# Performance work log

Hardware: AMD Instinct MI355X
Metric: run time of the kernel (lower is better)

Reference implementation:

```python
import jax, jax.numpy as jnp
import numpy as np

N_NODES = 10000
N_EDGES = 50000
DIM = 32
NHEAD = 4
HEAD_DIM = DIM // NHEAD
LN_EPS = 1e-5


def setup_inputs() -> dict:
    key = jax.random.key(0)
    ks = jax.random.split(key, 16)
    E, N, H, HD, D = N_EDGES, N_NODES, NHEAD, HEAD_DIM, DIM
    s = 1.0 / np.sqrt(D)
    return {
        "in_feat": jax.random.normal(ks[0], (N, D), jnp.float32),
        "src": jax.random.randint(ks[1], (E,), 0, N, jnp.int32),
        "dst": jax.random.randint(ks[2], (E,), 0, N, jnp.int32),
        "src_key_w": jax.random.normal(ks[3], (E, H, HD, D), jnp.float32) * s,
        "dst_key_w": jax.random.normal(ks[4], (E, H, HD, D), jnp.float32) * s,
        "src_key_b": jax.random.normal(ks[5], (E, H, HD), jnp.float32) * 0.02,
        "dst_key_b": jax.random.normal(ks[6], (E, H, HD), jnp.float32) * 0.02,
        "src_value_w": jax.random.normal(ks[7], (E, H, HD, D), jnp.float32) * s,
        "dst_value_w": jax.random.normal(ks[8], (E, H, HD, D), jnp.float32) * s,
        "src_value_b": jax.random.normal(ks[9], (E, H, HD), jnp.float32) * 0.02,
        "dst_value_b": jax.random.normal(ks[10], (E, H, HD), jnp.float32) * 0.02,
        "query": jax.random.normal(ks[11], (N, H, HD), jnp.float32) * s,
        "node_w": jax.random.normal(ks[12], (N, D, D), jnp.float32) * s,
        "node_b": jax.random.normal(ks[13], (N, D), jnp.float32) * 0.02,
        "ln_w": jnp.ones((D,), jnp.float32),
        "ln_b": jnp.zeros((D,), jnp.float32),
    }


def _layernorm(x, w, b):
    mu = jnp.mean(x, axis=-1, keepdims=True)
    var = jnp.mean(jnp.square(x - mu), axis=-1, keepdims=True)
    return (x - mu) * jax.lax.rsqrt(var + LN_EPS) * w + b


def reference(in_feat, src, dst, src_key_w, dst_key_w, src_key_b, dst_key_b,
              src_value_w, dst_value_w, src_value_b, dst_value_b,
              query, node_w, node_b, ln_w, ln_b):
    N = in_feat.shape[0]
    E = src.shape[0]
    u = in_feat[src]          # (E, D) source node feature per edge
    v = in_feat[dst]          # (E, D) destination node feature per edge

    # edgewise dynamic-weight linear: per-edge hypernetwork matmuls
    K = (jnp.einsum('ehdi,ei->ehd', src_key_w, u) + src_key_b
         + jnp.einsum('ehdi,ei->ehd', dst_key_w, v) + dst_key_b)   # (E, H, HD)
    V = (jnp.einsum('ehdi,ei->ehd', src_value_w, u) + src_value_b
         + jnp.einsum('ehdi,ei->ehd', dst_value_w, v) + dst_value_b)  # (E, H, HD)

    # e_dot_v(KEY, QUERY): per-edge per-head dot with dst-node query
    logits = jnp.einsum('ehd,ehd->eh', K, query[dst])  # (E, H)

    # edge_softmax over incoming edges of each dst node, per head
    m = jax.ops.segment_max(logits, dst, num_segments=N)   # (N, H)
    ex = jnp.exp(logits - m[dst])
    denom = jax.ops.segment_sum(ex, dst, num_segments=N)   # (N, H)
    attn = ex / denom[dst]                                  # (E, H)

    # weighted scatter-sum aggregation into dst nodes
    agg = jax.ops.segment_sum(V * attn[..., None], dst, num_segments=N)  # (N, H, HD)
    agg = agg.reshape(N, -1)  # (N, D)

    # nodewise dynamic linear + relu
    out = jnp.einsum('noi,ni->no', node_w, agg) + node_b
    out = jax.nn.relu(out)

    # residual + layernorm
    out = _layernorm(in_feat + out, ln_w, ln_b)

    key_feat = K.reshape(E, -1)
    value_feat = V.reshape(E, -1)
    return out, key_feat, value_feat, attn
```

## Files before the change

### kernel.cpp

```cpp
#include <hip/hip_runtime.h>
#include <math.h>

constexpr int N = 10000;
constexpr int E = 50000;
constexpr int D = 32;
constexpr int H = 4;

typedef float v4f __attribute__((ext_vector_type(4)));

__global__ __launch_bounds__(256) void hist_kernel(const int* __restrict__ dst,
                                                   int* __restrict__ counts)
{
    const int e = blockIdx.x * 256 + threadIdx.x;
    if (e < E) atomicAdd(counts + dst[e], 1);
}

__global__ __launch_bounds__(1024) void scan_kernel(const int* __restrict__ counts,
                                                    int* __restrict__ offsets,
                                                    int* __restrict__ cursor)
{
    __shared__ int part[1024];
    const int t = threadIdx.x;
    constexpr int PER = (N + 1023) / 1024;
    const int base = t * PER;
    int loc[PER];
    int s = 0;
    #pragma unroll
    for (int i = 0; i < PER; ++i) {
        const int c = (base + i < N) ? counts[base + i] : 0;
        loc[i] = s;
        s += c;
    }
    part[t] = s;
    __syncthreads();
    for (int off = 1; off < 1024; off <<= 1) {
        const int v = (t >= off) ? part[t - off] : 0;
        __syncthreads();
        part[t] += v;
        __syncthreads();
    }
    const int pre = (t == 0) ? 0 : part[t - 1];
    #pragma unroll
    for (int i = 0; i < PER; ++i) {
        if (base + i < N) {
            const int o = pre + loc[i];
            offsets[base + i] = o;
            cursor[base + i]  = o;
        }
    }
    if (t == 0) offsets[N] = E;
}

__global__ __launch_bounds__(256) void scatter_kernel(const int* __restrict__ dst,
                                                      int* __restrict__ cursor,
                                                      int* __restrict__ edge_list)
{
    const int e = blockIdx.x * 256 + threadIdx.x;
    if (e < E) {
        const int p = atomicAdd(cursor + dst[e], 1);
        edge_list[p] = e;
    }
}

__global__ __launch_bounds__(256) void edge_kernel(
    const float* __restrict__ in_feat,
    const int*   __restrict__ src, const int* __restrict__ dst,
    const float* __restrict__ skw, const float* __restrict__ dkw,
    const float* __restrict__ skb, const float* __restrict__ dkb,
    const float* __restrict__ svw, const float* __restrict__ dvw,
    const float* __restrict__ svb, const float* __restrict__ dvb,
    const float* __restrict__ query,
    float* __restrict__ key_feat, float* __restrict__ value_feat,
    float* __restrict__ ex_out)
{
    const int e   = blockIdx.x;
    const int tid = threadIdx.x;
    const int hd  = tid >> 3;
    const int seg = tid & 7;
    const int s = src[e];
    const int d = dst[e];

    const float4 u4 = *reinterpret_cast<const float4*>(in_feat + s * D + seg * 4);
    const float4 v4 = *reinterpret_cast<const float4*>(in_feat + d * D + seg * 4);

    const size_t woff = (size_t)e * 1024 + (size_t)tid * 4;
    const v4f wa = __builtin_nontemporal_load(reinterpret_cast<const v4f*>(skw + woff));
    const v4f wb = __builtin_nontemporal_load(reinterpret_cast<const v4f*>(dkw + woff));
    const v4f wc = __builtin_nontemporal_load(reinterpret_cast<const v4f*>(svw + woff));
    const v4f wd = __builtin_nontemporal_load(reinterpret_cast<const v4f*>(dvw + woff));

    float pk = wa.x * u4.x + wa.y * u4.y + wa.z * u4.z + wa.w * u4.w
             + wb.x * v4.x + wb.y * v4.y + wb.z * v4.z + wb.w * v4.w;
    float pv = wc.x * u4.x + wc.y * u4.y + wc.z * u4.z + wc.w * u4.w
             + wd.x * v4.x + wd.y * v4.y + wd.z * v4.z + wd.w * v4.w;

    #pragma unroll
    for (int off = 1; off < 8; off <<= 1) {
        pk += __shfl_xor(pk, off);
        pv += __shfl_xor(pv, off);
    }

    const int bi = e * D + hd;
    float c = 0.0f;
    if (seg == 0) {
        const float Kv = pk + skb[bi] + dkb[bi];
        const float Vv = pv + svb[bi] + dvb[bi];
        key_feat[bi]   = Kv;
        value_feat[bi] = Vv;
        c = Kv * query[d * D + hd];
    }
    #pragma unroll
    for (int off = 8; off < 64; off <<= 1) c += __shfl_xor(c, off);

    if ((tid & 63) == 0) {
        const int h = tid >> 6;
        ex_out[e * H + h] = expf(c);
    }
}

__global__ __launch_bounds__(256) void node_kernel(
    const int*   __restrict__ offsets, const int* __restrict__ edge_list,
    const float* __restrict__ in_feat, const float* __restrict__ value_feat,
    const float* __restrict__ node_w,  const float* __restrict__ node_b,
    const float* __restrict__ ln_w,    const float* __restrict__ ln_b,
    float* __restrict__ attn,
    float* __restrict__ out)
{
    __shared__ float agg_sh[4][33];
    const int wave = threadIdx.x >> 6;
    const int lane = threadIdx.x & 63;
    const int n = blockIdx.x * 4 + wave;

    const int beg = offsets[n];
    const int deg = offsets[n + 1] - beg;

    const int slot = lane >> 2;
    const int hh   = lane & 3;
    const int hd   = lane & 31;
    const int h    = hd >> 3;

    float ds = 0.0f;
    for (int k = slot; k < deg; k += 16)
        ds += attn[edge_list[beg + k] * H + hh];
    #pragma unroll
    for (int off = 4; off < 64; off <<= 1) ds += __shfl_xor(ds, off);
    const float rden = (ds != 0.0f) ? 1.0f / ds : 0.0f;

    float aggv = 0.0f;
    for (int c = 0; c < deg; c += 16) {
        const int rem = (deg - c < 16) ? (deg - c) : 16;
        int   ee = 0;
        float a  = 0.0f;
        if (slot < rem) {
            ee = edge_list[beg + c + slot];
            const int idx = ee * H + hh;
            a = attn[idx] * rden;
            attn[idx] = a;
        }
        for (int kk = 0; kk < rem; ++kk) {
            const float ak = __shfl(a, kk * 4 + h);
            const int  ek = __shfl(ee, kk * 4);
            aggv += value_feat[ek * D + hd] * ak;
        }
    }
    agg_sh[wave][hd] = aggv;
    __syncthreads();

    const int o = lane >> 1, half = lane & 1;
    const float* w = node_w + (size_t)n * 1024 + o * 32 + half * 16;
    const float* g = &agg_sh[wave][half * 16];
    float p = 0.0f;
    #pragma unroll
    for (int j = 0; j < 16; j += 4) {
        const float4 wv = *reinterpret_cast<const float4*>(w + j);
        p += wv.x * g[j] + wv.y * g[j + 1] + wv.z * g[j + 2] + wv.w * g[j + 3];
    }
    p += __shfl_xor(p, 1);

    const float r = in_feat[n * D + o] + fmaxf(p + node_b[n * D + o], 0.0f);

    float sum = r, sq = r * r;
    #pragma unroll
    for (int off = 2; off < 64; off <<= 1) {
        sum += __shfl_xor(sum, off);
        sq  += __shfl_xor(sq, off);
    }
    const float mean = sum * (1.0f / 32.0f);
    const float var  = sq * (1.0f / 32.0f) - mean * mean;
    const float y = (r - mean) * rsqrtf(var + 1e-5f) * ln_w[o] + ln_b[o];
    if (half == 0) out[n * D + o] = y;
}

extern "C" void kernel_launch(void* const* d_in, const int* in_sizes, int n_in,
                              void* d_out, int out_size, void* d_ws, size_t ws_size,
                              hipStream_t stream)
{
    const float* in_feat = (const float*)d_in[0];
    const int*   src     = (const int*)d_in[1];
    const int*   dst     = (const int*)d_in[2];
    const float* skw     = (const float*)d_in[3];
    const float* dkw     = (const float*)d_in[4];
    const float* skb     = (const float*)d_in[5];
    const float* dkb     = (const float*)d_in[6];
    const float* svw     = (const float*)d_in[7];
    const float* dvw     = (const float*)d_in[8];
    const float* svb     = (const float*)d_in[9];
    const float* dvb     = (const float*)d_in[10];
    const float* query   = (const float*)d_in[11];
    const float* node_w  = (const float*)d_in[12];
    const float* node_b  = (const float*)d_in[13];
    const float* ln_w    = (const float*)d_in[14];
    const float* ln_b    = (const float*)d_in[15];

    float* out        = (float*)d_out;
    float* key_feat   = out + (size_t)N * D;
    float* value_feat = key_feat + (size_t)E * D;
    float* attn       = value_feat + (size_t)E * D;

    int* counts    = (int*)d_ws;
    int* offsets   = counts + N;
    int* cursor    = offsets + (N + 1);
    int* edge_list = cursor + N;

    hipMemsetAsync(counts, 0, (size_t)N * sizeof(int), stream);
    hist_kernel<<<(E + 255) / 256, 256, 0, stream>>>(dst, counts);
    scan_kernel<<<1, 1024, 0, stream>>>(counts, offsets, cursor);
    scatter_kernel<<<(E + 255) / 256, 256, 0, stream>>>(dst, cursor, edge_list);

    edge_kernel<<<E, 256, 0, stream>>>(in_feat, src, dst,
                                       skw, dkw, skb, dkb,
                                       svw, dvw, svb, dvb,
                                       query, key_feat, value_feat, attn);

    node_kernel<<<N / 4, 256, 0, stream>>>(offsets, edge_list,
                                           in_feat, value_feat,
                                           node_w, node_b, ln_w, ln_b,
                                           attn, out);
}
```

Measured before the change: 705.3 us.

## Replace CSR build and gather with atomic scatter aggregation in edge kernel

The edge kernel now atomically accumulates exp(logit)*V into a per-node aggregation buffer (aliased onto the output region) and accumulates the softmax denominators per node and head. This removes the histogram, scan and scatter kernels and the per-node gather loop over incoming edges. Normalisation moves into the node kernel (dividing the aggregate by the denominator) and into a new small elementwise kernel that divides the stored attention weights. The trade-off is many float atomics to scattered destination nodes, plus summation order that is no longer deterministic.

```diff
diff --git a/kernel.cpp b/kernel.cpp
--- a/kernel.cpp
+++ b/kernel.cpp
@@ -8,60 +8,6 @@
 
 typedef float v4f __attribute__((ext_vector_type(4)));
 
-__global__ __launch_bounds__(256) void hist_kernel(const int* __restrict__ dst,
-                                                   int* __restrict__ counts)
-{
-    const int e = blockIdx.x * 256 + threadIdx.x;
-    if (e < E) atomicAdd(counts + dst[e], 1);
-}
-
-__global__ __launch_bounds__(1024) void scan_kernel(const int* __restrict__ counts,
-                                                    int* __restrict__ offsets,
-                                                    int* __restrict__ cursor)
-{
-    __shared__ int part[1024];
-    const int t = threadIdx.x;
-    constexpr int PER = (N + 1023) / 1024;
-    const int base = t * PER;
-    int loc[PER];
-    int s = 0;
-    #pragma unroll
-    for (int i = 0; i < PER; ++i) {
-        const int c = (base + i < N) ? counts[base + i] : 0;
-        loc[i] = s;
-        s += c;
-    }
-    part[t] = s;
-    __syncthreads();
-    for (int off = 1; off < 1024; off <<= 1) {
-        const int v = (t >= off) ? part[t - off] : 0;
-        __syncthreads();
-        part[t] += v;
-        __syncthreads();
-    }
-    const int pre = (t == 0) ? 0 : part[t - 1];
-    #pragma unroll
-    for (int i = 0; i < PER; ++i) {
-        if (base + i < N) {
-            const int o = pre + loc[i];
-            offsets[base + i] = o;
-            cursor[base + i]  = o;
-        }
-    }
-    if (t == 0) offsets[N] = E;
-}
-
-__global__ __launch_bounds__(256) void scatter_kernel(const int* __restrict__ dst,
-                                                      int* __restrict__ cursor,
-                                                      int* __restrict__ edge_list)
-{
-    const int e = blockIdx.x * 256 + threadIdx.x;
-    if (e < E) {
-        const int p = atomicAdd(cursor + dst[e], 1);
-        edge_list[p] = e;
-    }
-}
-
 __global__ __launch_bounds__(256) void edge_kernel(
     const float* __restrict__ in_feat,
     const int*   __restrict__ src, const int* __restrict__ dst,
@@ -71,7 +17,9 @@
     const float* __restrict__ svb, const float* __restrict__ dvb,
     const float* __restrict__ query,
     float* __restrict__ key_feat, float* __restrict__ value_feat,
-    float* __restrict__ ex_out)
+    float* __restrict__ ex_out,
+    float* __restrict__ aggU,
+    float* __restrict__ denom)
 {
     const int e   = blockIdx.x;
     const int tid = threadIdx.x;
@@ -101,10 +49,11 @@
     }
 
     const int bi = e * D + hd;
-    float c = 0.0f;
+    float c  = 0.0f;
+    float Vv = 0.0f;
     if (seg == 0) {
         const float Kv = pk + skb[bi] + dkb[bi];
-        const float Vv = pv + svb[bi] + dvb[bi];
+        Vv = pv + svb[bi] + dvb[bi];
         key_feat[bi]   = Kv;
         value_feat[bi] = Vv;
         c = Kv * query[d * D + hd];
@@ -112,18 +61,21 @@
     #pragma unroll
     for (int off = 8; off < 64; off <<= 1) c += __shfl_xor(c, off);
 
-    if ((tid & 63) == 0) {
-        const int h = tid >> 6;
-        ex_out[e * H + h] = expf(c);
+    if (seg == 0) {
+        const float ex = expf(c);
+        atomicAdd(aggU + d * D + hd, ex * Vv);
+        if ((tid & 63) == 0) {
+            const int h = tid >> 6;
+            ex_out[e * H + h] = ex;
+            atomicAdd(denom + d * H + h, ex);
+        }
     }
 }
 
 __global__ __launch_bounds__(256) void node_kernel(
-    const int*   __restrict__ offsets, const int* __restrict__ edge_list,
-    const float* __restrict__ in_feat, const float* __restrict__ value_feat,
+    const float* __restrict__ in_feat, const float* __restrict__ denom,
     const float* __restrict__ node_w,  const float* __restrict__ node_b,
     const float* __restrict__ ln_w,    const float* __restrict__ ln_b,
-    float* __restrict__ attn,
     float* __restrict__ out)
 {
     __shared__ float agg_sh[4][33];
@@ -131,39 +83,12 @@
     const int lane = threadIdx.x & 63;
     const int n = blockIdx.x * 4 + wave;
 
-    const int beg = offsets[n];
-    const int deg = offsets[n + 1] - beg;
+    const int hd = lane & 31;
+    const int h  = hd >> 3;
 
-    const int slot = lane >> 2;
-    const int hh   = lane & 3;
-    const int hd   = lane & 31;
-    const int h    = hd >> 3;
-
-    float ds = 0.0f;
-    for (int k = slot; k < deg; k += 16)
-        ds += attn[edge_list[beg + k] * H + hh];
-    #pragma unroll
-    for (int off = 4; off < 64; off <<= 1) ds += __shfl_xor(ds, off);
+    const float ds   = denom[n * H + h];
     const float rden = (ds != 0.0f) ? 1.0f / ds : 0.0f;
-
-    float aggv = 0.0f;
-    for (int c = 0; c < deg; c += 16) {
-        const int rem = (deg - c < 16) ? (deg - c) : 16;
-        int   ee = 0;
-        float a  = 0.0f;
-        if (slot < rem) {
-            ee = edge_list[beg + c + slot];
-            const int idx = ee * H + hh;
-            a = attn[idx] * rden;
-            attn[idx] = a;
-        }
-        for (int kk = 0; kk < rem; ++kk) {
-            const float ak = __shfl(a, kk * 4 + h);
-            const int  ek = __shfl(ee, kk * 4);
-            aggv += value_feat[ek * D + hd] * ak;
-        }
-    }
-    agg_sh[wave][hd] = aggv;
+    agg_sh[wave][hd] = out[n * D + hd] * rden;
     __syncthreads();
 
     const int o = lane >> 1, half = lane & 1;
@@ -189,6 +114,24 @@
     const float var  = sq * (1.0f / 32.0f) - mean * mean;
     const float y = (r - mean) * rsqrtf(var + 1e-5f) * ln_w[o] + ln_b[o];
     if (half == 0) out[n * D + o] = y;
+}
+
+__global__ __launch_bounds__(256) void attn_kernel(
+    const int* __restrict__ dst, const float* __restrict__ denom,
+    float* __restrict__ attn)
+{
+    const int e = blockIdx.x * 256 + threadIdx.x;
+    if (e < E) {
+        const int d = dst[e];
+        const float4 ex = *reinterpret_cast<const float4*>(attn + (size_t)e * H);
+        const float4 dn = *reinterpret_cast<const float4*>(denom + (size_t)d * H);
+        float4 r;
+        r.x = ex.x / dn.x;
+        r.y = ex.y / dn.y;
+        r.z = ex.z / dn.z;
+        r.w = ex.w / dn.w;
+        *reinterpret_cast<float4*>(attn + (size_t)e * H) = r;
+    }
 }
 
 extern "C" void kernel_launch(void* const* d_in, const int* in_sizes, int n_in,
@@ -217,23 +160,19 @@
     float* value_feat = key_feat + (size_t)E * D;
     float* attn       = value_feat + (size_t)E * D;
 
-    int* counts    = (int*)d_ws;
-    int* offsets   = counts + N;
-    int* cursor    = offsets + (N + 1);
-    int* edge_list = cursor + N;
+    float* denom = (float*)d_ws;
 
-    hipMemsetAsync(counts, 0, (size_t)N * sizeof(int), stream);
-    hist_kernel<<<(E + 255) / 256, 256, 0, stream>>>(dst, counts);
-    scan_kernel<<<1, 1024, 0, stream>>>(counts, offsets, cursor);
-    scatter_kernel<<<(E + 255) / 256, 256, 0, stream>>>(dst, cursor, edge_list);
+    hipMemsetAsync(out,   0, (size_t)N * D * sizeof(float), stream);
+    hipMemsetAsync(denom, 0, (size_t)N * H * sizeof(float), stream);
 
     edge_kernel<<<E, 256, 0, stream>>>(in_feat, src, dst,
                                        skw, dkw, skb, dkb,
                                        svw, dvw, svb, dvb,
-                                       query, key_feat, value_feat, attn);
+                                       query, key_feat, value_feat, attn,
+                                       out, denom);
 
-    node_kernel<<<N / 4, 256, 0, stream>>>(offsets, edge_list,
-                                           in_feat, value_feat,
-                                           node_w, node_b, ln_w, ln_b,
-                                           attn, out);
+    node_kernel<<<N / 4, 256, 0, stream>>>(in_feat, denom,
+                                           node_w, node_b, ln_w, ln_b, out);
+
+    attn_kernel<<<(E + 255) / 256, 256, 0, stream>>>(dst, denom, attn);
 }
```

Result: faster. 686.1 us (-2.7%).
